# Kernel optimization log

Measured on AMD Instinct MI355X. Metric: run time of the kernel, lower is better.

## Reference

```python
import jax, jax.numpy as jnp
import numpy as np

H, HK, D, BLK, GH = 32, 8, 96, 64, 128   # q heads, kv heads, head_dim, gate block, gate hidden
HIDDEN = 3072
THR = 0.03
NEG = -1e30

def _rot_half(x):
    h = x.shape[-1] // 2
    return jnp.concatenate([-x[..., h:], x[..., :h]], axis=-1)

def setup_inputs() -> dict:
    key = jax.random.key(0)
    ks = jax.random.split(key, 6)
    B, S = 1, 2048
    hidden_states = jax.random.normal(ks[0], (B, S, HIDDEN), dtype=jnp.float32)
    # RoPE tables, theta = 10000
    inv_freq = 1.0 / (10000.0 ** (np.arange(0, D, 2, dtype=np.float32) / D))
    t = np.arange(S, dtype=np.float32)
    freqs = np.outer(t, inv_freq)                   # [S, D/2]
    emb = np.concatenate([freqs, freqs], axis=-1)   # [S, D]
    cos = jnp.asarray(np.cos(emb), dtype=jnp.float32)
    sin = jnp.asarray(np.sin(emb), dtype=jnp.float32)
    op = H * D + 2 * HK * D
    qkv_w = jax.random.normal(ks[1], (HIDDEN, op), dtype=jnp.float32) * 0.02
    o_w = jax.random.normal(ks[2], (H * D, HIDDEN), dtype=jnp.float32) * 0.02
    gate_wq = jax.random.normal(ks[3], (D, GH), dtype=jnp.float32) * 0.05
    gate_wk = jax.random.normal(ks[4], (2 * D, GH), dtype=jnp.float32) * 0.05
    return dict(hidden_states=hidden_states, cos=cos, sin=sin,
                qkv_w=qkv_w, o_w=o_w, gate_wq=gate_wq, gate_wk=gate_wk)

def reference(hidden_states, cos, sin, qkv_w, o_w, gate_wq, gate_wk):
    B, S, _ = hidden_states.shape
    G = H // HK            # GQA group size
    nB = S // BLK          # number of gate blocks
    scale = D ** -0.5

    # fused QKV projection and head split
    qkv = hidden_states @ qkv_w
    q = qkv[..., : H * D].reshape(B, S, H, D)
    k = qkv[..., H * D : H * D + HK * D].reshape(B, S, HK, D)
    v = qkv[..., H * D + HK * D :].reshape(B, S, HK, D)
    q_nope, k_nope = q, k

    # RoPE (unsqueeze over head dim)
    cs = cos[None, :, None, :]
    sn = sin[None, :, None, :]
    q = q * cs + _rot_half(q) * sn
    k = k * cs + _rot_half(k) * sn

    # ---- learned block-sparse gate (SeerAttention AttnGate) ----
    kb = k_nope.reshape(B, nB, BLK, HK, D)
    k_pool = jnp.concatenate([kb.mean(2), kb.max(2)], axis=-1)      # [B,nB,HK,2D] avg+max seq pooling
    k_gate = jnp.einsum('bnhe,eg->bnhg', k_pool, gate_wk)
    q_pool = q_nope.reshape(B, S, HK, G, D).mean(3)                 # q-head pooling to kv heads
    q_pool = q_pool.reshape(B, nB, BLK, HK, D).mean(2)              # block pooling
    q_gate = jnp.einsum('bnhd,dg->bnhg', q_pool, gate_wq)
    gate_logits = jnp.einsum('bqhg,bkhg->bhqk', q_gate, k_gate) * (GH ** -0.5)
    blk_causal = jnp.tril(jnp.ones((nB, nB), dtype=bool))
    gate_logits = jnp.where(blk_causal, gate_logits, NEG)
    gate_probs = jax.nn.softmax(gate_logits, axis=-1)
    block_mask = (gate_probs >= THR) & blk_causal                   # threshold sparsity method
    block_mask = block_mask | jnp.eye(nB, dtype=bool)               # diagonal block always active

    # expand block mask to token level, intersect with causal mask
    tok_mask = jnp.repeat(jnp.repeat(block_mask, BLK, axis=2), BLK, axis=3)  # [B,HK,S,S]
    causal = jnp.tril(jnp.ones((S, S), dtype=bool))
    mask = tok_mask & causal

    # ---- block-sparse masked attention with GQA ----
    qh = q.transpose(0, 2, 1, 3).reshape(B, HK, G, S, D)
    kh = k.transpose(0, 2, 1, 3)                                    # [B,HK,S,D]
    vh = v.transpose(0, 2, 1, 3)
    scores = jnp.einsum('bhgsd,bhtd->bhgst', qh, kh) * scale
    scores = jnp.where(mask[:, :, None], scores, NEG)
    attn = jax.nn.softmax(scores, axis=-1)
    out = jnp.einsum('bhgst,bhtd->bhgsd', attn, vh)                 # [B,HK,G,S,D]
    out = out.reshape(B, H, S, D).transpose(0, 2, 1, 3).reshape(B, S, H * D)
    return out @ o_w
```

## Files before the change

kernel.cpp:

```cpp
#include <hip/hip_runtime.h>
#include <hip/hip_bf16.h>
#include <math.h>

#define S_LEN 2048
#define HID 3072
#define NHEAD 32
#define NKV 8
#define HDIM 96
#define QKV_N 4608
#define NB 32
#define GHDIM 128

typedef __attribute__((ext_vector_type(8))) short bf16x8;
typedef __attribute__((ext_vector_type(4))) float f32x4;
typedef unsigned short ushort_t;

#define SCALE2 0.14724444754f

__device__ __forceinline__ unsigned short f2bf(float x) {
    unsigned u = __float_as_uint(x);
    u += 0x7fffu + ((u >> 16) & 1u);
    return (unsigned short)(u >> 16);
}
__device__ __forceinline__ unsigned packbf2(float a, float b) {
    return (unsigned)f2bf(a) | ((unsigned)f2bf(b) << 16);
}

#define GLOBAL_AS __attribute__((address_space(1)))
#define LDS_AS __attribute__((address_space(3)))
__device__ __forceinline__ void gl_lds16(const void* g, void* l) {
    __builtin_amdgcn_global_load_lds((const GLOBAL_AS unsigned int*)g,
                                     (LDS_AS unsigned int*)l, 16, 0, 0);
}
__device__ __forceinline__ void barrier_raw() {
    asm volatile("s_barrier" ::: "memory");
}

__global__ __launch_bounds__(256, 2) void gemm_bf16(const ushort_t* __restrict__ A,
                                                    const ushort_t* __restrict__ Bt,
                                                    float* __restrict__ C,
                                                    int M, int N, int K) {
    __shared__ ushort_t As[128 * 64];
    __shared__ ushort_t Bs[128 * 64];
    const int tid = threadIdx.x;
    const int lane = tid & 63;
    const int w = tid >> 6;
    const int wm = (w >> 1) * 64;
    const int wn = (w & 1) * 64;
    const int l15 = lane & 15;
    const int quad = lane >> 4;
    const int m0 = blockIdx.y * 128;
    const int n0 = blockIdx.x * 128;

    f32x4 acc[4][4] = {};

    for (int k0 = 0; k0 < K; k0 += 64) {
        __syncthreads();
#pragma unroll
        for (int j = 0; j < 4; ++j) {
            int s = j * 256 + w * 64 + lane;
            int row = s >> 3;
            int kc = (s & 7) ^ (row & 7);
            gl_lds16(A + (size_t)(m0 + row) * K + k0 + kc * 8,
                     &As[(j * 256 + w * 64) * 8]);
        }
#pragma unroll
        for (int j = 0; j < 4; ++j) {
            int s = j * 256 + w * 64 + lane;
            int row = s >> 3;
            int kc = (s & 7) ^ (row & 7);
            gl_lds16(Bt + (size_t)(n0 + row) * K + k0 + kc * 8,
                     &Bs[(j * 256 + w * 64) * 8]);
        }
        __syncthreads();
        bf16x8 af[2][4], bf[2][4];
#pragma unroll
        for (int mt = 0; mt < 4; ++mt) {
            int row = wm + mt * 16 + l15;
            int rx = row & 7;
#pragma unroll
            for (int ph = 0; ph < 2; ++ph)
                af[ph][mt] = *(const bf16x8*)&As[(row * 8 + ((ph * 4 + quad) ^ rx)) * 8];
        }
#pragma unroll
        for (int nt = 0; nt < 4; ++nt) {
            int row = wn + nt * 16 + l15;
            int rx = row & 7;
#pragma unroll
            for (int ph = 0; ph < 2; ++ph)
                bf[ph][nt] = *(const bf16x8*)&Bs[(row * 8 + ((ph * 4 + quad) ^ rx)) * 8];
        }
#pragma unroll
        for (int ph = 0; ph < 2; ++ph)
#pragma unroll
            for (int mt = 0; mt < 4; ++mt)
#pragma unroll
                for (int nt = 0; nt < 4; ++nt)
                    acc[mt][nt] = __builtin_amdgcn_mfma_f32_16x16x32_bf16(
                        af[ph][mt], bf[ph][nt], acc[mt][nt], 0, 0, 0);
    }
#pragma unroll
    for (int mt = 0; mt < 4; ++mt)
#pragma unroll
        for (int nt = 0; nt < 4; ++nt)
#pragma unroll
            for (int r = 0; r < 4; ++r) {
                int row = m0 + wm + mt * 16 + quad * 4 + r;
                int col = n0 + wn + nt * 16 + l15;
                C[(size_t)row * N + col] = acc[mt][nt][r];
            }
}

__global__ __launch_bounds__(256) void conv_bf16(const float* __restrict__ X,
                                                 ushort_t* __restrict__ Y, int n4) {
    int i = blockIdx.x * 256 + threadIdx.x;
    if (i >= n4) return;
    const float4 v = *(const float4*)(X + (size_t)i * 4);
    int2 p;
    p.x = (int)packbf2(v.x, v.y);
    p.y = (int)packbf2(v.z, v.w);
    *(int2*)(Y + (size_t)i * 4) = p;
}

__global__ __launch_bounds__(256) void transpose_convert(const float* __restrict__ W,
                                                         ushort_t* __restrict__ Wt,
                                                         int K, int N) {
    __shared__ float Ts[64][65];
    const int k0 = blockIdx.y * 64, n0 = blockIdx.x * 64;
    const int tid = threadIdx.x;
    {
        int r = tid >> 2, cq = tid & 3;
#pragma unroll
        for (int i = 0; i < 4; ++i) {
            int c = cq * 16 + i * 4;
            const float4 v = *(const float4*)(W + (size_t)(k0 + r) * N + n0 + c);
            Ts[r][c] = v.x; Ts[r][c + 1] = v.y; Ts[r][c + 2] = v.z; Ts[r][c + 3] = v.w;
        }
    }
    __syncthreads();
#pragma unroll
    for (int it = 0; it < 2; ++it) {
        int n = (tid >> 3) + it * 32;
        int kc = tid & 7;
        int4 r;
        r.x = (int)(packbf2(Ts[kc * 8 + 0][n], Ts[kc * 8 + 1][n]));
        r.y = (int)(packbf2(Ts[kc * 8 + 2][n], Ts[kc * 8 + 3][n]));
        r.z = (int)(packbf2(Ts[kc * 8 + 4][n], Ts[kc * 8 + 5][n]));
        r.w = (int)(packbf2(Ts[kc * 8 + 6][n], Ts[kc * 8 + 7][n]));
        *(int4*)(Wt + (size_t)(n0 + n) * K + k0 + kc * 8) = r;
    }
}

__global__ __launch_bounds__(128) void pool_gate_k_kernel(const float* __restrict__ qkv,
                                                          const float* __restrict__ gate_wk,
                                                          float* __restrict__ k_gate) {
    int nb = blockIdx.x, h = blockIdx.y;
    int tid = threadIdx.x;
    __shared__ float pool[192];
    if (tid < 96) {
        float s = 0.f, mx = -1e30f;
        for (int i = 0; i < 64; i++) {
            float v = qkv[(size_t)(nb * 64 + i) * QKV_N + HID + h * 96 + tid];
            s += v;
            mx = fmaxf(mx, v);
        }
        pool[tid] = s * (1.f / 64.f);
        pool[96 + tid] = mx;
    }
    __syncthreads();
    float acc = 0.f;
    for (int e = 0; e < 192; e++) acc += pool[e] * gate_wk[e * GHDIM + tid];
    k_gate[(size_t)(nb * NKV + h) * GHDIM + tid] = acc;
}

__global__ __launch_bounds__(128) void pool_gate_q_kernel(const float* __restrict__ qkv,
                                                          const float* __restrict__ gate_wq,
                                                          float* __restrict__ q_gate) {
    int nb = blockIdx.x, h = blockIdx.y;
    int tid = threadIdx.x;
    __shared__ float pool[96];
    if (tid < 96) {
        float s = 0.f;
        for (int i = 0; i < 64; i++)
            for (int g = 0; g < 4; g++)
                s += qkv[(size_t)(nb * 64 + i) * QKV_N + (h * 4 + g) * 96 + tid];
        pool[tid] = s * (1.f / 256.f);
    }
    __syncthreads();
    float acc = 0.f;
    for (int e = 0; e < 96; e++) acc += pool[e] * gate_wq[e * GHDIM + tid];
    q_gate[(size_t)(nb * NKV + h) * GHDIM + tid] = acc;
}

__global__ __launch_bounds__(64) void blockmask_kernel(const float* __restrict__ q_gate,
                                                       const float* __restrict__ k_gate,
                                                       int* __restrict__ mask) {
    int h = blockIdx.x, qb = blockIdx.y;
    int tid = threadIdx.x;
    __shared__ float logits[32];
    if (tid < 32) {
        if (tid <= qb) {
            float acc = 0.f;
            const float* qg = &q_gate[(size_t)(qb * NKV + h) * GHDIM];
            const float* kg = &k_gate[(size_t)(tid * NKV + h) * GHDIM];
            for (int e = 0; e < GHDIM; e++) acc += qg[e] * kg[e];
            logits[tid] = acc * 0.08838834764831845f;
        } else {
            logits[tid] = -1e30f;
        }
    }
    __syncthreads();
    if (tid < 32) {
        float mx = -1e30f;
        for (int j = 0; j <= qb; j++) mx = fmaxf(mx, logits[j]);
        float sum = 0.f;
        for (int j = 0; j <= qb; j++) sum += __expf(logits[j] - mx);
        float p = (tid <= qb) ? __expf(logits[tid] - mx) / sum : 0.f;
        int m = ((p >= 0.03f) && (tid <= qb)) || (tid == qb);
        mask[(h * NB + qb) * NB + tid] = m;
    }
}

__global__ __launch_bounds__(256) void rope_qk_kernel(const float* __restrict__ qkv,
                                                      const float* __restrict__ cosb,
                                                      const float* __restrict__ sinb,
                                                      ushort_t* __restrict__ Qb,
                                                      ushort_t* __restrict__ Kb) {
    int idx = blockIdx.x * 256 + threadIdx.x;
    int d = idx % 48;
    int tmp = idx / 48;
    int head = tmp % 40;
    int s = tmp / 40;
    float c0 = cosb[s * 96 + d], c1 = cosb[s * 96 + d + 48];
    float s0 = sinb[s * 96 + d], s1 = sinb[s * 96 + d + 48];
    if (head < 32) {
        size_t base = (size_t)s * QKV_N + head * 96;
        float x0 = qkv[base + d], x1 = qkv[base + d + 48];
        size_t ob = (size_t)s * HID + head * 96;
        Qb[ob + d] = f2bf((x0 * c0 - x1 * s0) * SCALE2);
        Qb[ob + d + 48] = f2bf((x1 * c1 + x0 * s1) * SCALE2);
    } else {
        int hh = head - 32;
        size_t base = (size_t)s * QKV_N + HID + hh * 96;
        float x0 = qkv[base + d], x1 = qkv[base + d + 48];
        size_t ob = ((size_t)hh * S_LEN + s) * 96;
        Kb[ob + d] = f2bf(x0 * c0 - x1 * s0);
        Kb[ob + d + 48] = f2bf(x1 * c1 + x0 * s1);
    }
}

__global__ __launch_bounds__(256) void transpose_v_kernel(const float* __restrict__ qkv,
                                                          ushort_t* __restrict__ Vtb) {
    __shared__ float Vs[64][97];
    const int ibk = blockIdx.x, h = blockIdx.y;
    const int tid = threadIdx.x;
    {
        int t = tid >> 2, cq = tid & 3;
#pragma unroll
        for (int i = 0; i < 6; ++i) {
            int c = cq * 24 + i * 4;
            const float4 v = *(const float4*)(qkv + (size_t)(ibk * 64 + t) * QKV_N +
                                              HID + 768 + h * 96 + c);
            Vs[t][c] = v.x; Vs[t][c + 1] = v.y; Vs[t][c + 2] = v.z; Vs[t][c + 3] = v.w;
        }
    }
    __syncthreads();
#pragma unroll
    for (int it = 0; it < 3; ++it) {
        int s = tid + it * 256;
        int d = s >> 3, tc = s & 7;
        int4 r;
        r.x = (int)(packbf2(Vs[tc * 8 + 0][d], Vs[tc * 8 + 1][d]));
        r.y = (int)(packbf2(Vs[tc * 8 + 2][d], Vs[tc * 8 + 3][d]));
        r.z = (int)(packbf2(Vs[tc * 8 + 4][d], Vs[tc * 8 + 5][d]));
        r.w = (int)(packbf2(Vs[tc * 8 + 6][d], Vs[tc * 8 + 7][d]));
        *(int4*)(Vtb + ((size_t)h * 96 + d) * S_LEN + ibk * 64 + tc * 8) = r;
    }
}

__global__ __launch_bounds__(256) void attn_mfma(const ushort_t* __restrict__ Qb,
                                                 const ushort_t* __restrict__ Kb,
                                                 const ushort_t* __restrict__ Vtb,
                                                 const int* __restrict__ mask,
                                                 ushort_t* __restrict__ out) {
    const int hq = blockIdx.x;
    const int ib = NB - 1 - (int)blockIdx.y;
    const int h = hq >> 2;
    const int tid = threadIdx.x;
    const int lane = tid & 63;
    const int w = tid >> 6;
    const int l15 = lane & 15;
    const int quad = lane >> 4;

    __shared__ ushort_t KsL[2][64 * 96];
    __shared__ ushort_t VtL[2][96 * 64];
    __shared__ ushort_t Ps[64][72];

    int pk[3];
    {
        int b0 = quad + (l15 & 7);
#pragma unroll
        for (int ks = 0; ks < 3; ++ks) {
            int p = b0 + ks * 4;
            if (p >= 12) p -= 12;
            if (p >= 12) p -= 12;
            pk[ks] = p;
        }
    }

    bf16x8 qf[3];
    {
        const ushort_t* qp = Qb + (size_t)(ib * 64 + w * 16 + l15) * HID + hq * 96;
#pragma unroll
        for (int ks = 0; ks < 3; ++ks)
            qf[ks] = *(const bf16x8*)(qp + ks * 32 + quad * 8);
    }

    const ushort_t* kbase = Kb + (size_t)h * S_LEN * 96;
    const ushort_t* vbase = Vtb + (size_t)h * 96 * S_LEN;

    unsigned long long bits =
        __ballot((lane <= ib) && (mask[(h * NB + ib) * NB + (lane & 31)] != 0));

    float m_i[4], l_i[4];
#pragma unroll
    for (int r = 0; r < 4; ++r) { m_i[r] = -1e30f; l_i[r] = 0.f; }
    f32x4 acc_o[6] = {};

    auto stage = [&](int jb, int buf) {
#pragma unroll
        for (int j = 0; j < 3; ++j) {
            int s = j * 256 + w * 64 + lane;
            int t = (s * 2731) >> 15;
            int cpos = s - t * 12;
            int c = cpos - (t & 7);
            if (c < 0) c += 12;
            gl_lds16(kbase + (size_t)(jb * 64 + t) * 96 + c * 8,
                     &KsL[buf][(j * 256 + w * 64) * 8]);
        }
#pragma unroll
        for (int j = 0; j < 3; ++j) {
            int s = j * 256 + w * 64 + lane;
            int d = s >> 3;
            int tc = (s & 7) ^ (d & 7);
            gl_lds16(vbase + (size_t)d * S_LEN + jb * 64 + tc * 8,
                     &VtL[buf][(j * 256 + w * 64) * 8]);
        }
    };

    int jb = (int)__builtin_ctzll(bits);
    bits &= bits - 1;
    stage(jb, 0);
    int cur = 0;

    while (true) {
        int jn = -1;
        if (bits) {
            jn = (int)__builtin_ctzll(bits);
            bits &= bits - 1;
        }
        if (jn >= 0) {
            stage(jn, cur ^ 1);
            asm volatile("s_waitcnt vmcnt(6)" ::: "memory");
        } else {
            asm volatile("s_waitcnt vmcnt(0)" ::: "memory");
        }
        barrier_raw();

        const ushort_t* Kc = KsL[cur];
        const ushort_t* Vc = VtL[cur];

        f32x4 s4[4] = {};
#pragma unroll
        for (int ks = 0; ks < 3; ++ks)
#pragma unroll
            for (int nt = 0; nt < 4; ++nt) {
                bf16x8 kb = *(const bf16x8*)&Kc[(nt * 16 + l15) * 96 + pk[ks] * 8];
                s4[nt] = __builtin_amdgcn_mfma_f32_16x16x32_bf16(qf[ks], kb, s4[nt], 0, 0, 0);
            }
        if (jb == ib) {
#pragma unroll
            for (int nt = 0; nt < 4; ++nt)
#pragma unroll
                for (int r = 0; r < 4; ++r)
                    if ((nt * 16 + l15) > (w * 16 + quad * 4 + r)) s4[nt][r] = -1e30f;
        }
        float alpha[4];
#pragma unroll
        for (int r = 0; r < 4; ++r) {
            float mx = fmaxf(fmaxf(s4[0][r], s4[1][r]), fmaxf(s4[2][r], s4[3][r]));
            mx = fmaxf(mx, __shfl_xor(mx, 1));
            mx = fmaxf(mx, __shfl_xor(mx, 2));
            mx = fmaxf(mx, __shfl_xor(mx, 4));
            mx = fmaxf(mx, __shfl_xor(mx, 8));
            float mnew = fmaxf(m_i[r], mx);
            alpha[r] = __builtin_amdgcn_exp2f(m_i[r] - mnew);
            float ps = 0.f;
#pragma unroll
            for (int nt = 0; nt < 4; ++nt) {
                float p = __builtin_amdgcn_exp2f(s4[nt][r] - mnew);
                s4[nt][r] = p;
                ps += p;
            }
            ps += __shfl_xor(ps, 1);
            ps += __shfl_xor(ps, 2);
            ps += __shfl_xor(ps, 4);
            ps += __shfl_xor(ps, 8);
            l_i[r] = l_i[r] * alpha[r] + ps;
            m_i[r] = mnew;
        }
#pragma unroll
        for (int t = 0; t < 6; ++t)
#pragma unroll
            for (int r = 0; r < 4; ++r) acc_o[t][r] *= alpha[r];
#pragma unroll
        for (int nt = 0; nt < 4; ++nt)
#pragma unroll
            for (int r = 0; r < 4; ++r)
                Ps[w * 16 + quad * 4 + r][nt * 16 + l15] = (short)f2bf(s4[nt][r]);
#pragma unroll
        for (int ks = 0; ks < 2; ++ks) {
            bf16x8 pa = *(const bf16x8*)&Ps[w * 16 + l15][ks * 32 + quad * 8];
#pragma unroll
            for (int t = 0; t < 6; ++t) {
                int d = t * 16 + l15;
                int slot = (ks * 4 + quad) ^ (d & 7);
                bf16x8 vb = *(const bf16x8*)&Vc[(d * 8 + slot) * 8];
                acc_o[t] = __builtin_amdgcn_mfma_f32_16x16x32_bf16(pa, vb, acc_o[t], 0, 0, 0);
            }
        }

        if (jn < 0) break;
        asm volatile("s_waitcnt lgkmcnt(0)" ::: "memory");
        barrier_raw();
        jb = jn;
        cur ^= 1;
    }

#pragma unroll
    for (int r = 0; r < 4; ++r) {
        float inv = 1.f / l_i[r];
        int row = ib * 64 + w * 16 + quad * 4 + r;
#pragma unroll
        for (int t = 0; t < 6; ++t)
            out[(size_t)row * HID + hq * 96 + t * 16 + l15] = f2bf(acc_o[t][r] * inv);
    }
}

extern "C" void kernel_launch(void* const* d_in, const int* in_sizes, int n_in,
                              void* d_out, int out_size, void* d_ws, size_t ws_size,
                              hipStream_t stream) {
    const float* hidden  = (const float*)d_in[0];
    const float* cosb    = (const float*)d_in[1];
    const float* sinb    = (const float*)d_in[2];
    const float* qkv_w   = (const float*)d_in[3];
    const float* o_w     = (const float*)d_in[4];
    const float* gate_wq = (const float*)d_in[5];
    const float* gate_wk = (const float*)d_in[6];
    float* out = (float*)d_out;

    char* ws = (char*)d_ws;
    float*    qkv   = (float*)ws;
    ushort_t* h_bf  = (ushort_t*)(ws + 37748736);
    ushort_t* w1t   = (ushort_t*)(ws + 50331648);
    ushort_t* attn_out = (ushort_t*)(ws + 78643200);
    ushort_t* Kb    = (ushort_t*)(ws + 91226112);
    ushort_t* Vtb   = (ushort_t*)(ws + 95420416);
    float* k_gate   = (float*)(ws + 98566144);
    float* q_gate   = (float*)(ws + 98697216);
    int*   mask     = (int*)(ws + 98828288);
    ushort_t* Qb    = h_bf;
    ushort_t* o_wt  = (ushort_t*)qkv;

    conv_bf16<<<(S_LEN * HID / 4 + 255) / 256, 256, 0, stream>>>(hidden, h_bf, S_LEN * HID / 4);
    transpose_convert<<<dim3(QKV_N / 64, HID / 64), 256, 0, stream>>>(qkv_w, w1t, HID, QKV_N);
    gemm_bf16<<<dim3(QKV_N / 128, S_LEN / 128), 256, 0, stream>>>(h_bf, w1t, qkv, S_LEN, QKV_N, HID);
    pool_gate_k_kernel<<<dim3(NB, NKV), 128, 0, stream>>>(qkv, gate_wk, k_gate);
    pool_gate_q_kernel<<<dim3(NB, NKV), 128, 0, stream>>>(qkv, gate_wq, q_gate);
    blockmask_kernel<<<dim3(NKV, NB), 64, 0, stream>>>(q_gate, k_gate, mask);
    rope_qk_kernel<<<S_LEN * 40 * 48 / 256, 256, 0, stream>>>(qkv, cosb, sinb, Qb, Kb);
    transpose_v_kernel<<<dim3(NB, NKV), 256, 0, stream>>>(qkv, Vtb);
    transpose_convert<<<dim3(HID / 64, HID / 64), 256, 0, stream>>>(o_w, o_wt, HID, HID);
    attn_mfma<<<dim3(NHEAD, NB), 256, 0, stream>>>(Qb, Kb, Vtb, mask, attn_out);
    gemm_bf16<<<dim3(HID / 128, S_LEN / 128), 256, 0, stream>>>(attn_out, o_wt, out, S_LEN, HID, HID);
}
```

Before: 413.9 us.

## Compute transposed S tile so P feeds PV MFMA from registers, dropping LDS round-trip

Swaps the MFMA operand order so the score tile is produced transposed: each lane holds one query row's scores across key positions. The row max and sum then need only two cross-lane shuffles, and the probabilities can be packed straight into bf16x4 operands for 16x16x16 MFMAs computing O^T = V^T P^T. This removes the shared-memory P buffer, its store/load and the shuffle-heavy per-row reductions. In exchange it uses the smaller 16x16x16 MFMA, issuing more instructions per PV product, and switches to packed 8-byte output stores.

```diff
diff --git a/kernel.cpp b/kernel.cpp
--- a/kernel.cpp
+++ b/kernel.cpp
@@ -12,6 +12,7 @@
 #define GHDIM 128
 
 typedef __attribute__((ext_vector_type(8))) short bf16x8;
+typedef __attribute__((ext_vector_type(4))) short bf16x4;
 typedef __attribute__((ext_vector_type(4))) float f32x4;
 typedef unsigned short ushort_t;
 
@@ -294,7 +295,6 @@
 
     __shared__ ushort_t KsL[2][64 * 96];
     __shared__ ushort_t VtL[2][96 * 64];
-    __shared__ ushort_t Ps[64][72];
 
     int pk[3];
     {
@@ -322,9 +322,7 @@
     unsigned long long bits =
         __ballot((lane <= ib) && (mask[(h * NB + ib) * NB + (lane & 31)] != 0));
 
-    float m_i[4], l_i[4];
-#pragma unroll
-    for (int r = 0; r < 4; ++r) { m_i[r] = -1e30f; l_i[r] = 0.f; }
+    float m_i = -1e30f, l_i = 0.f;
     f32x4 acc_o[6] = {};
 
     auto stage = [&](int jb, int buf) {
@@ -370,63 +368,66 @@
         const ushort_t* Kc = KsL[cur];
         const ushort_t* Vc = VtL[cur];
 
-        f32x4 s4[4] = {};
+        f32x4 st[4] = {};
 #pragma unroll
         for (int ks = 0; ks < 3; ++ks)
 #pragma unroll
             for (int nt = 0; nt < 4; ++nt) {
                 bf16x8 kb = *(const bf16x8*)&Kc[(nt * 16 + l15) * 96 + pk[ks] * 8];
-                s4[nt] = __builtin_amdgcn_mfma_f32_16x16x32_bf16(qf[ks], kb, s4[nt], 0, 0, 0);
+                st[nt] = __builtin_amdgcn_mfma_f32_16x16x32_bf16(kb, qf[ks], st[nt], 0, 0, 0);
             }
         if (jb == ib) {
+            int q = w * 16 + l15;
 #pragma unroll
             for (int nt = 0; nt < 4; ++nt)
 #pragma unroll
                 for (int r = 0; r < 4; ++r)
-                    if ((nt * 16 + l15) > (w * 16 + quad * 4 + r)) s4[nt][r] = -1e30f;
-        }
-        float alpha[4];
-#pragma unroll
-        for (int r = 0; r < 4; ++r) {
-            float mx = fmaxf(fmaxf(s4[0][r], s4[1][r]), fmaxf(s4[2][r], s4[3][r]));
-            mx = fmaxf(mx, __shfl_xor(mx, 1));
-            mx = fmaxf(mx, __shfl_xor(mx, 2));
-            mx = fmaxf(mx, __shfl_xor(mx, 4));
-            mx = fmaxf(mx, __shfl_xor(mx, 8));
-            float mnew = fmaxf(m_i[r], mx);
-            alpha[r] = __builtin_amdgcn_exp2f(m_i[r] - mnew);
-            float ps = 0.f;
-#pragma unroll
-            for (int nt = 0; nt < 4; ++nt) {
-                float p = __builtin_amdgcn_exp2f(s4[nt][r] - mnew);
-                s4[nt][r] = p;
+                    if ((nt * 16 + quad * 4 + r) > q) st[nt][r] = -1e30f;
+        }
+        float mx = -1e30f;
+#pragma unroll
+        for (int nt = 0; nt < 4; ++nt)
+#pragma unroll
+            for (int r = 0; r < 4; ++r) mx = fmaxf(mx, st[nt][r]);
+        mx = fmaxf(mx, __shfl_xor(mx, 16));
+        mx = fmaxf(mx, __shfl_xor(mx, 32));
+        float mnew = fmaxf(m_i, mx);
+        float alpha = __builtin_amdgcn_exp2f(m_i - mnew);
+        float ps = 0.f;
+#pragma unroll
+        for (int nt = 0; nt < 4; ++nt)
+#pragma unroll
+            for (int r = 0; r < 4; ++r) {
+                float p = __builtin_amdgcn_exp2f(st[nt][r] - mnew);
+                st[nt][r] = p;
                 ps += p;
             }
-            ps += __shfl_xor(ps, 1);
-            ps += __shfl_xor(ps, 2);
-            ps += __shfl_xor(ps, 4);
-            ps += __shfl_xor(ps, 8);
-            l_i[r] = l_i[r] * alpha[r] + ps;
-            m_i[r] = mnew;
-        }
+        ps += __shfl_xor(ps, 16);
+        ps += __shfl_xor(ps, 32);
+        l_i = l_i * alpha + ps;
+        m_i = mnew;
 #pragma unroll
         for (int t = 0; t < 6; ++t)
 #pragma unroll
-            for (int r = 0; r < 4; ++r) acc_o[t][r] *= alpha[r];
-#pragma unroll
-        for (int nt = 0; nt < 4; ++nt)
-#pragma unroll
-            for (int r = 0; r < 4; ++r)
-                Ps[w * 16 + quad * 4 + r][nt * 16 + l15] = (short)f2bf(s4[nt][r]);
-#pragma unroll
-        for (int ks = 0; ks < 2; ++ks) {
-            bf16x8 pa = *(const bf16x8*)&Ps[w * 16 + l15][ks * 32 + quad * 8];
-#pragma unroll
-            for (int t = 0; t < 6; ++t) {
-                int d = t * 16 + l15;
-                int slot = (ks * 4 + quad) ^ (d & 7);
-                bf16x8 vb = *(const bf16x8*)&Vc[(d * 8 + slot) * 8];
-                acc_o[t] = __builtin_amdgcn_mfma_f32_16x16x32_bf16(pa, vb, acc_o[t], 0, 0, 0);
+            for (int r = 0; r < 4; ++r) acc_o[t][r] *= alpha;
+        bf16x4 pf[4];
+#pragma unroll
+        for (int kblk = 0; kblk < 4; ++kblk) {
+            union { bf16x4 v; unsigned u[2]; } pb;
+            pb.u[0] = packbf2(st[kblk][0], st[kblk][1]);
+            pb.u[1] = packbf2(st[kblk][2], st[kblk][3]);
+            pf[kblk] = pb.v;
+        }
+#pragma unroll
+        for (int kblk = 0; kblk < 4; ++kblk) {
+            int cchunk = kblk * 2 + (quad >> 1);
+            int eoff = (quad & 1) * 4;
+#pragma unroll
+            for (int dt = 0; dt < 6; ++dt) {
+                int d = dt * 16 + l15;
+                bf16x4 vf = *(const bf16x4*)&Vc[(d * 8 + (cchunk ^ (d & 7))) * 8 + eoff];
+                acc_o[dt] = __builtin_amdgcn_mfma_f32_16x16x16bf16_1k(
+                    vf, pf[kblk], acc_o[dt], 0, 0, 0);
             }
         }
 
@@ -437,13 +438,14 @@
         cur ^= 1;
     }
 
-#pragma unroll
-    for (int r = 0; r < 4; ++r) {
-        float inv = 1.f / l_i[r];
-        int row = ib * 64 + w * 16 + quad * 4 + r;
-#pragma unroll
-        for (int t = 0; t < 6; ++t)
-            out[(size_t)row * HID + hq * 96 + t * 16 + l15] = f2bf(acc_o[t][r] * inv);
+    float inv = 1.f / l_i;
+    size_t orow = (size_t)(ib * 64 + w * 16 + l15) * HID + hq * 96;
+#pragma unroll
+    for (int dt = 0; dt < 6; ++dt) {
+        int2 pkd;
+        pkd.x = (int)packbf2(acc_o[dt][0] * inv, acc_o[dt][1] * inv);
+        pkd.y = (int)packbf2(acc_o[dt][2] * inv, acc_o[dt][3] * inv);
+        *(int2*)(out + orow + dt * 16 + quad * 4) = pkd;
     }
 }
 
```

After: 389.2 us. 6.0% less time.
